# Performance work log

Hardware: AMD Instinct MI355X
Metric: run time of the kernel (lower is better)

Reference implementation:

```python
import jax, jax.numpy as jnp
import numpy as np

# module hyper-params (from init_kwargs)
NMS_THRESHOLD = 0.45
CLASSES = 32        # number of classes to filter
PRE_THRESHOLD = 0.005
FIRST_CLASS = 0

B, N, C = 8, 2048, 32  # batch, boxes-per-image, total class channels


def setup_inputs() -> dict:
    key = jax.random.key(0)
    k1, k2, k3 = jax.random.split(key, 3)
    # boxes in (x1, y1, x2, y2) corner format with positive extent
    cxy = jax.random.uniform(k1, (B, N, 2), dtype=jnp.float32) * 100.0
    wh = jax.random.uniform(k2, (B, N, 2), dtype=jnp.float32) * 20.0 + 1.0
    bbs = jnp.concatenate([cxy - wh * 0.5, cxy + wh * 0.5], axis=-1)  # [B,N,4]
    conf = jax.random.uniform(k3, (B, C, N), dtype=jnp.float32)       # [B,C,N]
    return {"bbs": bbs, "conf": conf}


def _iou_matrix(boxes):
    # boxes: [N,4] (x1,y1,x2,y2) -> pairwise IoU [N,N]
    lt = jnp.maximum(boxes[:, None, :2], boxes[None, :, :2])
    rb = jnp.minimum(boxes[:, None, 2:], boxes[None, :, 2:])
    wh = jnp.clip(rb - lt, 0.0)
    inter = wh[..., 0] * wh[..., 1]
    area = (boxes[:, 2] - boxes[:, 0]) * (boxes[:, 3] - boxes[:, 1])
    union = area[:, None] + area[None, :] - inter
    return inter / jnp.maximum(union, jnp.float32(1e-12))


def _nms_one_class(iou, conf_c):
    # iou: [N,N] pairwise IoU for this image; conf_c: [N] confidences of one class.
    # Greedy NMS in descending confidence order; suppressed boxes get conf 0.
    if PRE_THRESHOLD > 0:
        conf_c = jnp.where(conf_c > PRE_THRESHOLD, conf_c, 0.0)
    order = jnp.argsort(-conf_c)          # descending
    conf_s = conf_c[order]                # sorted confidences
    idx = jnp.arange(N)

    def step(suppressed, i):
        # suppressed[i] is final at step i (only earlier steps could set it)
        active = (~suppressed[i]) & (conf_s[i] > 0)
        row = iou[order[i]][order]        # IoU of box i (sorted order) vs all, sorted
        suppressed = suppressed | (active & (row > NMS_THRESHOLD) & (idx > i))
        return suppressed, suppressed[i] if False else suppressed[i]

    def step2(suppressed, i):
        sup_i = suppressed[i]
        active = (~sup_i) & (conf_s[i] > 0)
        row = iou[order[i]][order]
        new_sup = suppressed | (active & (row > NMS_THRESHOLD) & (idx > i))
        return new_sup, sup_i

    _, sup_at = jax.lax.scan(step2, jnp.zeros((N,), dtype=bool), idx)
    out_s = jnp.where(sup_at, 0.0, conf_s)
    return jnp.zeros((N,), conf_c.dtype).at[order].set(out_s)


def reference(bbs, conf):
    # bbs [B,N,4], conf [B,C,N] -> filtered conf [B,C,N]
    iou = jax.vmap(_iou_matrix)(bbs)  # [B,N,N]
    nms_bc = jax.vmap(lambda io, cf: jax.vmap(lambda c: _nms_one_class(io, c))(cf))(iou, conf)
    cls = jnp.arange(conf.shape[1])
    in_range = (cls >= FIRST_CLASS) & (cls < FIRST_CLASS + CLASSES)
    # classes outside [first_class, first_class+classes) pass through unchanged
    return jnp.where(in_range[None, :, None], nms_bc, conf)
```

## Files before the change

kernel.cpp:

```cpp
#include <hip/hip_runtime.h>
#include <stdint.h>

#pragma clang fp contract(off)

#define BB   8
#define NN   2048
#define CC   32
#define WORDS 64
#define NBLK 64
#define NMS_THR 0.45f
#define PRE_THR 0.005f
#define PADI(i) ((((i) >> 5) * 33) + ((i) & 31))
#define KPAD(i) ((i) + ((i) >> 4))

typedef unsigned long long u64;

__global__ __launch_bounds__(256) void adj_kernel(const float* __restrict__ bbs,
                                                  uint32_t* __restrict__ adj) {
    __shared__ float2 sA[2112];
    __shared__ float2 sB[2112];
    const int b = blockIdx.y;
    const int t = threadIdx.x;
    const float4* bp = (const float4*)bbs + (size_t)b * NN;
    for (int i = t; i < NN; i += 256) {
        float4 v = bp[i];
        int p = PADI(i);
        sA[p] = make_float2(v.x, v.y);
        sB[p] = make_float2(v.z, v.w);
    }
    __syncthreads();

    const int wave = t >> 6, lane = t & 63;
    const int row0 = blockIdx.x * 16 + wave * 4;
    const double M = (double)0.45f + 0x1p-26;

    float ax1[4], ay1[4], ax2[4], ay2[4], areaA[4];
#pragma unroll
    for (int r = 0; r < 4; ++r) {
        int p = PADI(row0 + r);
        float2 a = sA[p], bz = sB[p];
        ax1[r] = a.x; ay1[r] = a.y; ax2[r] = bz.x; ay2[r] = bz.y;
        areaA[r] = (bz.x - a.x) * (bz.y - a.y);
    }
    uint32_t w[4] = {0, 0, 0, 0};
#pragma unroll
    for (int j = 0; j < 32; ++j) {
        int p = lane * 33 + j;
        float2 a = sA[p], bz = sB[p];
        float areaB = (bz.x - a.x) * (bz.y - a.y);
#pragma unroll
        for (int r = 0; r < 4; ++r) {
            float ltx = fmaxf(ax1[r], a.x),  lty = fmaxf(ay1[r], a.y);
            float rbx = fminf(ax2[r], bz.x), rby = fminf(ay2[r], bz.y);
            float ww = fmaxf(rbx - ltx, 0.0f);
            float hh = fmaxf(rby - lty, 0.0f);
            float inter = ww * hh;
            float uni  = (areaA[r] + areaB) - inter;
            float unim = fmaxf(uni, 1e-12f);
            bool adjb = (double)inter > M * (double)unim;
            w[r] |= adjb ? (1u << j) : 0u;
        }
    }
#pragma unroll
    for (int r = 0; r < 4; ++r) {
        int row = row0 + r;
        uint32_t dmask = (lane == (row >> 5)) ? ~(1u << (row & 31)) : 0xFFFFFFFFu;
        adj[((size_t)b * NN + row) * WORDS + lane] = w[r] & dmask;
    }
}

__device__ __forceinline__ void ce_reg(u64& a, u64& b, bool up) {
    u64 mn = (a < b) ? a : b;
    u64 mx = (a < b) ? b : a;
    a = up ? mx : mn;
    b = up ? mn : mx;
}

__global__ __launch_bounds__(1024) void sort_kernel(const float* __restrict__ conf,
                                                    uint32_t* __restrict__ wsOrd) {
    __shared__ u64 keys[2176];
    const int bc = blockIdx.x;
    const int t  = threadIdx.x;
    const float* cf = conf + (size_t)bc * NN;

    if (t < 512) {
        const int g = 4 * t;
        float4 v = ((const float4*)cf)[t];
        float f0 = (v.x > PRE_THR) ? v.x : 0.0f;
        float f1 = (v.y > PRE_THR) ? v.y : 0.0f;
        float f2 = (v.z > PRE_THR) ? v.z : 0.0f;
        float f3 = (v.w > PRE_THR) ? v.w : 0.0f;
        u64 a0 = ((u64)__float_as_uint(f0) << 32) | (uint32_t)(NN - 1 - (g + 0));
        u64 a1 = ((u64)__float_as_uint(f1) << 32) | (uint32_t)(NN - 1 - (g + 1));
        u64 a2 = ((u64)__float_as_uint(f2) << 32) | (uint32_t)(NN - 1 - (g + 2));
        u64 a3 = ((u64)__float_as_uint(f3) << 32) | (uint32_t)(NN - 1 - (g + 3));
        ce_reg(a0, a1, true);
        ce_reg(a2, a3, false);
        bool up4 = ((g & 4) == 0);
        ce_reg(a0, a2, up4); ce_reg(a1, a3, up4);
        ce_reg(a0, a1, up4); ce_reg(a2, a3, up4);
        keys[KPAD(g + 0)] = a0; keys[KPAD(g + 1)] = a1;
        keys[KPAD(g + 2)] = a2; keys[KPAD(g + 3)] = a3;
    }
    __syncthreads();

    for (unsigned k = 8; k <= NN; k <<= 1) {
        unsigned j = k >> 1;
        while (j >= 2) {
            const unsigned h = j >> 1;
            if (t < 512) {
                unsigned g  = (((unsigned)t & ~(h - 1)) << 2) | ((unsigned)t & (h - 1));
                bool up = ((g & k) == 0);
                u64 e0 = keys[KPAD(g)];
                u64 e1 = keys[KPAD(g + h)];
                u64 e2 = keys[KPAD(g + j)];
                u64 e3 = keys[KPAD(g + j + h)];
                ce_reg(e0, e2, up); ce_reg(e1, e3, up);
                ce_reg(e0, e1, up); ce_reg(e2, e3, up);
                keys[KPAD(g)]         = e0;
                keys[KPAD(g + h)]     = e1;
                keys[KPAD(g + j)]     = e2;
                keys[KPAD(g + j + h)] = e3;
            }
            __syncthreads();
            j >>= 2;
        }
        if (j == 1) {
            unsigned i  = (unsigned)t << 1;
            bool up = ((i & k) == 0);
            u64 a = keys[KPAD(i)], d = keys[KPAD(i + 1)];
            ce_reg(a, d, up);
            keys[KPAD(i)] = a; keys[KPAD(i + 1)] = d;
            __syncthreads();
        }
    }

    uint32_t* ov = wsOrd + (size_t)bc * NN;
    for (int r = t; r < NN; r += 1024) {
        u64 kk = keys[KPAD(r)];
        uint32_t idx = (uint32_t)(NN - 1) - (uint32_t)(kk & 0xffffffffu);
        uint32_t nz  = ((uint32_t)(kk >> 32) != 0u) ? 0x10000u : 0u;
        ov[r] = idx | nz;
    }
}

__global__ __launch_bounds__(256) void extract_kernel(const uint32_t* __restrict__ adj,
                                                      const uint32_t* __restrict__ wsOrd,
                                                      uint32_t* __restrict__ wsM) {
    const int blkid = blockIdx.x;
    const int bc = blkid >> 3, chunk = blkid & 7;
    const int b  = bc >> 5;
    const int t = threadIdx.x, wv = t >> 6, lane = t & 63, e = lane & 31, h = lane >> 5;
    const uint32_t* ov = wsOrd + (size_t)bc * NN;
    const uint32_t* ab = adj + (size_t)b * NN * WORDS;

    for (int blk = chunk * 8 + wv; blk < chunk * 8 + 8; blk += 4) {
        uint32_t ue = ov[blk * 32 + e];
        int widx = (int)((ue & 0xffffu) >> 5);
        int bpos = (int)(ue & 31u);
        uint32_t wb[16];
#pragma unroll
        for (int k = 0; k < 16; ++k) {
            uint32_t ud = ov[blk * 32 + k * 2 + h] & 0xffffu;
            wb[k] = ab[(size_t)ud * WORDS + widx];
        }
        uint32_t vM = 0;
#pragma unroll
        for (int k = 0; k < 16; ++k) {
            unsigned long long bal = __ballot(((wb[k] >> bpos) & 1u) != 0u);
            vM = (lane == 2 * k    ) ? (uint32_t)bal         : vM;
            vM = (lane == 2 * k + 1) ? (uint32_t)(bal >> 32) : vM;
        }
        if (lane < 32)
            wsM[(size_t)bc * NN + blk * 32 + lane] = vM & (0xFFFFFFFEu << lane);
    }
}

__global__ __launch_bounds__(256) void scan_kernel(const float* __restrict__ conf,
                                                   const uint32_t* __restrict__ adj,
                                                   const uint32_t* __restrict__ wsOrd,
                                                   const uint32_t* __restrict__ wsM,
                                                   float* __restrict__ out) {
    __shared__ uint32_t buf[2][256][64];
    __shared__ uint32_t ordL[NN];
    __shared__ uint32_t Ml[NN];
    __shared__ uint32_t Sarr[WORDS];
    const int bc = blockIdx.x;
    const int b  = bc >> 5;
    const int t  = threadIdx.x, wid = t >> 6, lane = t & 63;
    const uint32_t* ov = wsOrd + (size_t)bc * NN;
    const uint32_t* mv = wsM   + (size_t)bc * NN;
    const uint32_t* ab = adj + (size_t)b * NN * WORDS;
    const float* cf = conf + (size_t)bc * NN;
    float* op = out + (size_t)bc * NN;

    for (int i = t; i < NN; i += 256) { ordL[i] = ov[i]; Ml[i] = mv[i]; }
    __syncthreads();

    for (int r = wid; r < 256; r += 4) {
        uint32_t ud = ordL[r] & 0xffffu;
        buf[0][r][lane] = ab[(size_t)ud * WORDS + lane];
    }
    __syncthreads();

    uint32_t S = 0;
    for (int c = 0; c < 8; ++c) {
        const int cb = c & 1, nb = cb ^ 1;
        if (wid != 0) {
            if (c < 7) {
                const int base = (c + 1) * 256;
                for (int r = wid - 1; r < 256; r += 3) {
                    uint32_t ud = ordL[base + r] & 0xffffu;
                    buf[nb][r][lane] = ab[(size_t)ud * WORDS + lane];
                }
            }
        } else {
            for (int k = 0; k < 8; ++k) {
                const int blk = c * 8 + k;
                uint32_t u = ordL[blk * 32 + (lane & 31)];
                uint32_t m = Ml[blk * 32 + (lane & 31)];
                int wq = (int)(((u & 0xffffu) >> 5) << 2);
                int pm = __builtin_amdgcn_ds_bpermute(wq, (int)S);
                uint32_t rw[32];
#pragma unroll
                for (int d = 0; d < 32; ++d)
                    rw[d] = buf[cb][k * 32 + d][lane];
                bool a0 = (((u >> 16) & 1u) != 0u) && (((pm >> (u & 31u)) & 1) == 0);
                uint32_t alive = (uint32_t)__ballot((int)a0);
                if (alive) {
#pragma unroll
                    for (int d = 0; d < 32; ++d) {
                        uint32_t mk = (uint32_t)__builtin_amdgcn_readlane((int)m, d);
                        alive = (alive & (1u << d)) ? (alive & ~mk) : alive;
                    }
                    uint32_t acc = 0;
#pragma unroll
                    for (int d = 0; d < 32; ++d)
                        acc |= (alive & (1u << d)) ? rw[d] : 0u;
                    S |= acc;
                }
            }
        }
        __syncthreads();
    }
    if (wid == 0) Sarr[lane] = S;
    __syncthreads();

#pragma unroll 2
    for (int i = t; i < NN; i += 256) {
        float v = cf[i];
        bool sup = (Sarr[i >> 5] >> (i & 31)) & 1u;
        op[i] = (v > PRE_THR && !sup) ? v : 0.0f;
    }
}

__global__ __launch_bounds__(256) void nms_fallback(const float* __restrict__ conf,
                                                    const uint32_t* __restrict__ adj,
                                                    float* __restrict__ out) {
    __shared__ unsigned long long keys[NN];
    __shared__ uint32_t ordv[NN];
    __shared__ uint32_t Mlds[NBLK * 32];
    __shared__ uint32_t Sarr[WORDS];
    const int bc = blockIdx.x;
    const int b  = bc >> 5;
    const int t  = threadIdx.x;
    const float* cf = conf + (size_t)bc * NN;
    const uint32_t* const abase = adj + (size_t)b * NN * WORDS;

    for (int i = t; i < NN; i += 256) {
        float v  = cf[i];
        float vt = (v > PRE_THR) ? v : 0.0f;
        keys[i] = ((unsigned long long)__float_as_uint(vt) << 32) | (uint32_t)(NN - 1 - i);
    }
    __syncthreads();
    for (unsigned k = 2; k <= NN; k <<= 1)
        for (unsigned j = k >> 1; j > 0; j >>= 1) {
            for (unsigned p = t; p < NN / 2; p += 256) {
                unsigned i  = ((p & ~(j - 1)) << 1) | (p & (j - 1));
                unsigned ij = i | j;
                unsigned long long a = keys[i], d = keys[ij];
                bool up = ((i & k) == 0);
                if (up ? (a < d) : (a > d)) { keys[i] = d; keys[ij] = a; }
            }
            __syncthreads();
        }
    for (int r = t; r < NN; r += 256) {
        unsigned long long kk = keys[r];
        uint32_t idx = (uint32_t)(NN - 1) - (uint32_t)(kk & 0xffffffffu);
        uint32_t nz  = ((uint32_t)(kk >> 32) != 0u) ? 0x10000u : 0u;
        ordv[r] = idx | nz;
    }
    __syncthreads();
    {
        const int wid = t >> 6, lane = t & 63, e = lane & 31, h = lane >> 5;
        for (int blk = wid * 16; blk < wid * 16 + 16; ++blk) {
            uint32_t ue = ordv[blk * 32 + e];
            int widx = (int)((ue & 0xffffu) >> 5);
            int bpos = (int)(ue & 31u);
            uint32_t vM = 0;
#pragma unroll
            for (int half = 0; half < 2; ++half) {
                uint32_t wbuf[8];
#pragma unroll
                for (int k = 0; k < 8; ++k) {
                    int d = half * 16 + k * 2 + h;
                    uint32_t ud = ordv[blk * 32 + d] & 0xffffu;
                    wbuf[k] = abase[(size_t)ud * WORDS + widx];
                }
#pragma unroll
                for (int k = 0; k < 8; ++k) {
                    int d0 = half * 16 + k * 2;
                    unsigned long long bal = __ballot(((wbuf[k] >> bpos) & 1u) != 0u);
                    vM = (lane == d0    ) ? (uint32_t)bal         : vM;
                    vM = (lane == d0 + 1) ? (uint32_t)(bal >> 32) : vM;
                }
            }
            if (lane < 32) Mlds[blk * 32 + lane] = vM;
        }
    }
    __syncthreads();
    if (t < 64) {
        const int lane = t;
        const uint32_t* const rowp = abase + lane;
        uint32_t S = 0;
        uint32_t rbA[32], rbB[32];
        uint32_t u_c, m_c, u_n, m_n;
        u_c = ordv[lane & 31];
        m_c = Mlds[lane & 31];
#pragma unroll
        for (int d = 0; d < 32; ++d) {
            int ud = __builtin_amdgcn_readlane((int)u_c, d) & 0xffff;
            rbA[d] = rowp[(size_t)ud * WORDS];
        }
        auto do_block = [&](int blk, uint32_t (&rbC)[32], uint32_t (&rbN)[32]) {
            u_n = 0; m_n = 0;
            if (blk < 63) {
                u_n = ordv[(blk + 1) * 32 + (lane & 31)];
                m_n = Mlds[(blk + 1) * 32 + (lane & 31)];
#pragma unroll
                for (int d = 0; d < 32; ++d) {
                    int ud = __builtin_amdgcn_readlane((int)u_n, d) & 0xffff;
                    rbN[d] = rowp[(size_t)ud * WORDS];
                }
            }
            int wq  = (int)(((u_c & 0xffffu) >> 5) << 2);
            int bpv = (int)(u_c & 31u);
            int pm  = __builtin_amdgcn_ds_bpermute(wq, (int)S);
            bool a0 = (((u_c >> 16) & 1u) != 0u) && (((pm >> bpv) & 1) == 0);
            uint32_t alive = (uint32_t)__ballot((int)a0);
#pragma unroll
            for (int d = 0; d < 32; ++d) {
                uint32_t rowd = (uint32_t)__builtin_amdgcn_readlane((int)m_c, d);
                uint32_t mk = rowd & (0xFFFFFFFEu << d);
                alive = (alive & (1u << d)) ? (alive & ~mk) : alive;
            }
            uint32_t acc = 0;
#pragma unroll
            for (int d = 0; d < 32; ++d)
                acc |= (alive & (1u << d)) ? rbC[d] : 0u;
            S |= acc;
            u_c = u_n; m_c = m_n;
        };
        for (int blk = 0; blk < 64; blk += 2) {
            do_block(blk,     rbA, rbB);
            do_block(blk + 1, rbB, rbA);
        }
        Sarr[lane] = S;
    }
    __syncthreads();
    float* op = out + (size_t)bc * NN;
    for (int i = t; i < NN; i += 256) {
        float v = cf[i];
        bool sup = (Sarr[i >> 5] >> (i & 31)) & 1u;
        op[i] = (v > PRE_THR && !sup) ? v : 0.0f;
    }
}

extern "C" void kernel_launch(void* const* d_in, const int* in_sizes, int n_in,
                              void* d_out, int out_size, void* d_ws, size_t ws_size,
                              hipStream_t stream) {
    const float* bbs  = (const float*)d_in[0];
    const float* conf = (const float*)d_in[1];
    float* out = (float*)d_out;

    const size_t adjB = (size_t)BB * NN * WORDS * sizeof(uint32_t);
    const size_t ordB = (size_t)BB * CC * NN * sizeof(uint32_t);
    const size_t mB   = ordB;
    uint32_t* adj = (uint32_t*)d_ws;

    if (ws_size >= adjB + ordB + mB) {
        uint32_t* wsOrd = (uint32_t*)((char*)d_ws + adjB);
        uint32_t* wsM   = (uint32_t*)((char*)d_ws + adjB + ordB);
        adj_kernel    <<<dim3(NN / 16, BB), 256, 0, stream>>>(bbs, adj);
        sort_kernel   <<<BB * CC, 1024, 0, stream>>>(conf, wsOrd);
        extract_kernel<<<BB * CC * 8, 256, 0, stream>>>(adj, wsOrd, wsM);
        scan_kernel   <<<BB * CC, 256, 0, stream>>>(conf, adj, wsOrd, wsM, out);
    } else if (ws_size >= adjB) {
        adj_kernel  <<<dim3(NN / 16, BB), 256, 0, stream>>>(bbs, adj);
        nms_fallback<<<BB * CC, 256, 0, stream>>>(conf, adj, out);
    }
}
```

Measured before the change: 165.8 us.

## Fuse sort, mask extraction and greedy scan into one 512-thread kernel

Merges the separate sort, extract and scan kernels into a single kernel per (batch, class) with 512 threads. The sort keys alias the scan's double buffer in shared memory, and the order and mask arrays stay in LDS instead of going through global workspace. Prefetch now runs on seven warps and the final write is vectorized to float4. This removes two kernel launches and the global round trips for order and mask. In exchange it drops the 8-way chunked parallelism of the extract stage, leaving only 256 blocks in total, and removes the fallback path.

```diff
diff --git a/kernel.cpp b/kernel.cpp
--- a/kernel.cpp
+++ b/kernel.cpp
@@ -76,14 +76,23 @@
     b = up ? mn : mx;
 }
 
-__global__ __launch_bounds__(1024) void sort_kernel(const float* __restrict__ conf,
-                                                    uint32_t* __restrict__ wsOrd) {
-    __shared__ u64 keys[2176];
+__global__ __launch_bounds__(512, 1) void nms_fused(const float* __restrict__ conf,
+                                                    const uint32_t* __restrict__ adj,
+                                                    float* __restrict__ out) {
+    __shared__ uint32_t buf[2][256][64];
+    __shared__ uint32_t ordL[NN];
+    __shared__ uint32_t Ml[NN];
+    __shared__ uint32_t Sarr[WORDS];
+    u64* keys = (u64*)&buf[0][0][0];
+
     const int bc = blockIdx.x;
-    const int t  = threadIdx.x;
+    const int b  = bc >> 5;
+    const int t  = threadIdx.x, wid = t >> 6, lane = t & 63;
     const float* cf = conf + (size_t)bc * NN;
-
-    if (t < 512) {
+    const uint32_t* ab = adj + (size_t)b * NN * WORDS;
+    float* op = out + (size_t)bc * NN;
+
+    {
         const int g = 4 * t;
         float4 v = ((const float4*)cf)[t];
         float f0 = (v.x > PRE_THR) ? v.x : 0.0f;
@@ -108,7 +117,7 @@
         unsigned j = k >> 1;
         while (j >= 2) {
             const unsigned h = j >> 1;
-            if (t < 512) {
+            {
                 unsigned g  = (((unsigned)t & ~(h - 1)) << 2) | ((unsigned)t & (h - 1));
                 bool up = ((g & k) == 0);
                 u64 e0 = keys[KPAD(g)];
@@ -126,78 +135,52 @@
             j >>= 2;
         }
         if (j == 1) {
-            unsigned i  = (unsigned)t << 1;
-            bool up = ((i & k) == 0);
-            u64 a = keys[KPAD(i)], d = keys[KPAD(i + 1)];
-            ce_reg(a, d, up);
-            keys[KPAD(i)] = a; keys[KPAD(i + 1)] = d;
+#pragma unroll
+            for (int it = 0; it < 2; ++it) {
+                unsigned i = ((unsigned)t + it * 512u) << 1;
+                bool up = ((i & k) == 0);
+                u64 a = keys[KPAD(i)], d = keys[KPAD(i + 1)];
+                ce_reg(a, d, up);
+                keys[KPAD(i)] = a; keys[KPAD(i + 1)] = d;
+            }
             __syncthreads();
         }
     }
 
-    uint32_t* ov = wsOrd + (size_t)bc * NN;
-    for (int r = t; r < NN; r += 1024) {
+    for (int r = t; r < NN; r += 512) {
         u64 kk = keys[KPAD(r)];
         uint32_t idx = (uint32_t)(NN - 1) - (uint32_t)(kk & 0xffffffffu);
         uint32_t nz  = ((uint32_t)(kk >> 32) != 0u) ? 0x10000u : 0u;
-        ov[r] = idx | nz;
-    }
-}
-
-__global__ __launch_bounds__(256) void extract_kernel(const uint32_t* __restrict__ adj,
-                                                      const uint32_t* __restrict__ wsOrd,
-                                                      uint32_t* __restrict__ wsM) {
-    const int blkid = blockIdx.x;
-    const int bc = blkid >> 3, chunk = blkid & 7;
-    const int b  = bc >> 5;
-    const int t = threadIdx.x, wv = t >> 6, lane = t & 63, e = lane & 31, h = lane >> 5;
-    const uint32_t* ov = wsOrd + (size_t)bc * NN;
-    const uint32_t* ab = adj + (size_t)b * NN * WORDS;
-
-    for (int blk = chunk * 8 + wv; blk < chunk * 8 + 8; blk += 4) {
-        uint32_t ue = ov[blk * 32 + e];
-        int widx = (int)((ue & 0xffffu) >> 5);
-        int bpos = (int)(ue & 31u);
-        uint32_t wb[16];
-#pragma unroll
-        for (int k = 0; k < 16; ++k) {
-            uint32_t ud = ov[blk * 32 + k * 2 + h] & 0xffffu;
-            wb[k] = ab[(size_t)ud * WORDS + widx];
-        }
-        uint32_t vM = 0;
-#pragma unroll
-        for (int k = 0; k < 16; ++k) {
-            unsigned long long bal = __ballot(((wb[k] >> bpos) & 1u) != 0u);
-            vM = (lane == 2 * k    ) ? (uint32_t)bal         : vM;
-            vM = (lane == 2 * k + 1) ? (uint32_t)(bal >> 32) : vM;
-        }
-        if (lane < 32)
-            wsM[(size_t)bc * NN + blk * 32 + lane] = vM & (0xFFFFFFFEu << lane);
-    }
-}
-
-__global__ __launch_bounds__(256) void scan_kernel(const float* __restrict__ conf,
-                                                   const uint32_t* __restrict__ adj,
-                                                   const uint32_t* __restrict__ wsOrd,
-                                                   const uint32_t* __restrict__ wsM,
-                                                   float* __restrict__ out) {
-    __shared__ uint32_t buf[2][256][64];
-    __shared__ uint32_t ordL[NN];
-    __shared__ uint32_t Ml[NN];
-    __shared__ uint32_t Sarr[WORDS];
-    const int bc = blockIdx.x;
-    const int b  = bc >> 5;
-    const int t  = threadIdx.x, wid = t >> 6, lane = t & 63;
-    const uint32_t* ov = wsOrd + (size_t)bc * NN;
-    const uint32_t* mv = wsM   + (size_t)bc * NN;
-    const uint32_t* ab = adj + (size_t)b * NN * WORDS;
-    const float* cf = conf + (size_t)bc * NN;
-    float* op = out + (size_t)bc * NN;
-
-    for (int i = t; i < NN; i += 256) { ordL[i] = ov[i]; Ml[i] = mv[i]; }
-    __syncthreads();
-
-    for (int r = wid; r < 256; r += 4) {
+        ordL[r] = idx | nz;
+    }
+    __syncthreads();
+
+    {
+        const int e = lane & 31, h = lane >> 5;
+        for (int blk = wid * 8; blk < wid * 8 + 8; ++blk) {
+            uint32_t ue = ordL[blk * 32 + e];
+            int widx = (int)((ue & 0xffffu) >> 5);
+            int bpos = (int)(ue & 31u);
+            uint32_t wb[16];
+#pragma unroll
+            for (int k = 0; k < 16; ++k) {
+                uint32_t ud = ordL[blk * 32 + k * 2 + h] & 0xffffu;
+                wb[k] = ab[(size_t)ud * WORDS + widx];
+            }
+            uint32_t vM = 0;
+#pragma unroll
+            for (int k = 0; k < 16; ++k) {
+                unsigned long long bal = __ballot(((wb[k] >> bpos) & 1u) != 0u);
+                vM = (lane == 2 * k    ) ? (uint32_t)bal         : vM;
+                vM = (lane == 2 * k + 1) ? (uint32_t)(bal >> 32) : vM;
+            }
+            if (lane < 32)
+                Ml[blk * 32 + lane] = vM & (0xFFFFFFFEu << lane);
+        }
+    }
+    __syncthreads();
+
+    for (int r = wid; r < 256; r += 8) {
         uint32_t ud = ordL[r] & 0xffffu;
         buf[0][r][lane] = ab[(size_t)ud * WORDS + lane];
     }
@@ -209,7 +192,7 @@
         if (wid != 0) {
             if (c < 7) {
                 const int base = (c + 1) * 256;
-                for (int r = wid - 1; r < 256; r += 3) {
+                for (int r = wid - 1; r < 256; r += 7) {
                     uint32_t ud = ordL[base + r] & 0xffffu;
                     buf[nb][r][lane] = ab[(size_t)ud * WORDS + lane];
                 }
@@ -246,133 +229,16 @@
     if (wid == 0) Sarr[lane] = S;
     __syncthreads();
 
-#pragma unroll 2
-    for (int i = t; i < NN; i += 256) {
-        float v = cf[i];
-        bool sup = (Sarr[i >> 5] >> (i & 31)) & 1u;
-        op[i] = (v > PRE_THR && !sup) ? v : 0.0f;
-    }
-}
-
-__global__ __launch_bounds__(256) void nms_fallback(const float* __restrict__ conf,
-                                                    const uint32_t* __restrict__ adj,
-                                                    float* __restrict__ out) {
-    __shared__ unsigned long long keys[NN];
-    __shared__ uint32_t ordv[NN];
-    __shared__ uint32_t Mlds[NBLK * 32];
-    __shared__ uint32_t Sarr[WORDS];
-    const int bc = blockIdx.x;
-    const int b  = bc >> 5;
-    const int t  = threadIdx.x;
-    const float* cf = conf + (size_t)bc * NN;
-    const uint32_t* const abase = adj + (size_t)b * NN * WORDS;
-
-    for (int i = t; i < NN; i += 256) {
-        float v  = cf[i];
-        float vt = (v > PRE_THR) ? v : 0.0f;
-        keys[i] = ((unsigned long long)__float_as_uint(vt) << 32) | (uint32_t)(NN - 1 - i);
-    }
-    __syncthreads();
-    for (unsigned k = 2; k <= NN; k <<= 1)
-        for (unsigned j = k >> 1; j > 0; j >>= 1) {
-            for (unsigned p = t; p < NN / 2; p += 256) {
-                unsigned i  = ((p & ~(j - 1)) << 1) | (p & (j - 1));
-                unsigned ij = i | j;
-                unsigned long long a = keys[i], d = keys[ij];
-                bool up = ((i & k) == 0);
-                if (up ? (a < d) : (a > d)) { keys[i] = d; keys[ij] = a; }
-            }
-            __syncthreads();
-        }
-    for (int r = t; r < NN; r += 256) {
-        unsigned long long kk = keys[r];
-        uint32_t idx = (uint32_t)(NN - 1) - (uint32_t)(kk & 0xffffffffu);
-        uint32_t nz  = ((uint32_t)(kk >> 32) != 0u) ? 0x10000u : 0u;
-        ordv[r] = idx | nz;
-    }
-    __syncthreads();
     {
-        const int wid = t >> 6, lane = t & 63, e = lane & 31, h = lane >> 5;
-        for (int blk = wid * 16; blk < wid * 16 + 16; ++blk) {
-            uint32_t ue = ordv[blk * 32 + e];
-            int widx = (int)((ue & 0xffffu) >> 5);
-            int bpos = (int)(ue & 31u);
-            uint32_t vM = 0;
-#pragma unroll
-            for (int half = 0; half < 2; ++half) {
-                uint32_t wbuf[8];
-#pragma unroll
-                for (int k = 0; k < 8; ++k) {
-                    int d = half * 16 + k * 2 + h;
-                    uint32_t ud = ordv[blk * 32 + d] & 0xffffu;
-                    wbuf[k] = abase[(size_t)ud * WORDS + widx];
-                }
-#pragma unroll
-                for (int k = 0; k < 8; ++k) {
-                    int d0 = half * 16 + k * 2;
-                    unsigned long long bal = __ballot(((wbuf[k] >> bpos) & 1u) != 0u);
-                    vM = (lane == d0    ) ? (uint32_t)bal         : vM;
-                    vM = (lane == d0 + 1) ? (uint32_t)(bal >> 32) : vM;
-                }
-            }
-            if (lane < 32) Mlds[blk * 32 + lane] = vM;
-        }
-    }
-    __syncthreads();
-    if (t < 64) {
-        const int lane = t;
-        const uint32_t* const rowp = abase + lane;
-        uint32_t S = 0;
-        uint32_t rbA[32], rbB[32];
-        uint32_t u_c, m_c, u_n, m_n;
-        u_c = ordv[lane & 31];
-        m_c = Mlds[lane & 31];
-#pragma unroll
-        for (int d = 0; d < 32; ++d) {
-            int ud = __builtin_amdgcn_readlane((int)u_c, d) & 0xffff;
-            rbA[d] = rowp[(size_t)ud * WORDS];
-        }
-        auto do_block = [&](int blk, uint32_t (&rbC)[32], uint32_t (&rbN)[32]) {
-            u_n = 0; m_n = 0;
-            if (blk < 63) {
-                u_n = ordv[(blk + 1) * 32 + (lane & 31)];
-                m_n = Mlds[(blk + 1) * 32 + (lane & 31)];
-#pragma unroll
-                for (int d = 0; d < 32; ++d) {
-                    int ud = __builtin_amdgcn_readlane((int)u_n, d) & 0xffff;
-                    rbN[d] = rowp[(size_t)ud * WORDS];
-                }
-            }
-            int wq  = (int)(((u_c & 0xffffu) >> 5) << 2);
-            int bpv = (int)(u_c & 31u);
-            int pm  = __builtin_amdgcn_ds_bpermute(wq, (int)S);
-            bool a0 = (((u_c >> 16) & 1u) != 0u) && (((pm >> bpv) & 1) == 0);
-            uint32_t alive = (uint32_t)__ballot((int)a0);
-#pragma unroll
-            for (int d = 0; d < 32; ++d) {
-                uint32_t rowd = (uint32_t)__builtin_amdgcn_readlane((int)m_c, d);
-                uint32_t mk = rowd & (0xFFFFFFFEu << d);
-                alive = (alive & (1u << d)) ? (alive & ~mk) : alive;
-            }
-            uint32_t acc = 0;
-#pragma unroll
-            for (int d = 0; d < 32; ++d)
-                acc |= (alive & (1u << d)) ? rbC[d] : 0u;
-            S |= acc;
-            u_c = u_n; m_c = m_n;
-        };
-        for (int blk = 0; blk < 64; blk += 2) {
-            do_block(blk,     rbA, rbB);
-            do_block(blk + 1, rbB, rbA);
-        }
-        Sarr[lane] = S;
-    }
-    __syncthreads();
-    float* op = out + (size_t)bc * NN;
-    for (int i = t; i < NN; i += 256) {
-        float v = cf[i];
-        bool sup = (Sarr[i >> 5] >> (i & 31)) & 1u;
-        op[i] = (v > PRE_THR && !sup) ? v : 0.0f;
+        int i4 = t * 4;
+        float4 v = ((const float4*)cf)[t];
+        uint32_t sw = Sarr[i4 >> 5];
+        float4 o;
+        o.x = (v.x > PRE_THR && !((sw >> ((i4 + 0) & 31)) & 1u)) ? v.x : 0.0f;
+        o.y = (v.y > PRE_THR && !((sw >> ((i4 + 1) & 31)) & 1u)) ? v.y : 0.0f;
+        o.z = (v.z > PRE_THR && !((sw >> ((i4 + 2) & 31)) & 1u)) ? v.z : 0.0f;
+        o.w = (v.w > PRE_THR && !((sw >> ((i4 + 3) & 31)) & 1u)) ? v.w : 0.0f;
+        ((float4*)op)[t] = o;
     }
 }
 
@@ -384,19 +250,9 @@
     float* out = (float*)d_out;
 
     const size_t adjB = (size_t)BB * NN * WORDS * sizeof(uint32_t);
-    const size_t ordB = (size_t)BB * CC * NN * sizeof(uint32_t);
-    const size_t mB   = ordB;
     uint32_t* adj = (uint32_t*)d_ws;
-
-    if (ws_size >= adjB + ordB + mB) {
-        uint32_t* wsOrd = (uint32_t*)((char*)d_ws + adjB);
-        uint32_t* wsM   = (uint32_t*)((char*)d_ws + adjB + ordB);
-        adj_kernel    <<<dim3(NN / 16, BB), 256, 0, stream>>>(bbs, adj);
-        sort_kernel   <<<BB * CC, 1024, 0, stream>>>(conf, wsOrd);
-        extract_kernel<<<BB * CC * 8, 256, 0, stream>>>(adj, wsOrd, wsM);
-        scan_kernel   <<<BB * CC, 256, 0, stream>>>(conf, adj, wsOrd, wsM, out);
-    } else if (ws_size >= adjB) {
-        adj_kernel  <<<dim3(NN / 16, BB), 256, 0, stream>>>(bbs, adj);
-        nms_fallback<<<BB * CC, 256, 0, stream>>>(conf, adj, out);
-    }
-}
+    if (ws_size < adjB) return;
+
+    adj_kernel<<<dim3(NN / 16, BB), 256, 0, stream>>>(bbs, adj);
+    nms_fused <<<BB * CC, 512, 0, stream>>>(conf, adj, out);
+}
```

Result: faster. 156.7 us (-5.5%).
